# Performance work log

Measured on AMD Instinct MI355X. Metric: run time of the kernel, lower is better.

The kernel has to match this reference:

```python
import jax, jax.numpy as jnp
import numpy as np

N_NODES = 50000


def setup_inputs() -> dict:
    key = jax.random.key(0)
    k1, k2, k3, k4 = jax.random.split(key, 4)
    N, E, D_IN, D_OUT = N_NODES, 1_600_000, 128, 128
    x = jax.random.normal(k1, (N, D_IN), dtype=jnp.float32)
    edge_index = jax.random.randint(k2, (2, E), 0, N, dtype=jnp.int64)
    W = jax.random.normal(k3, (D_IN, D_OUT), dtype=jnp.float32) * (1.0 / np.sqrt(D_IN))
    b = jax.random.normal(k4, (D_OUT,), dtype=jnp.float32) * 0.01
    return {"x": x, "edge_index": edge_index, "W": W, "b": b}


def reference(x, edge_index, W, b):
    N = x.shape[0]
    # add self loops: edge (i, i) for every node
    loops = jnp.arange(N, dtype=edge_index.dtype)
    row = jnp.concatenate([edge_index[0], loops])  # [E+N]
    col = jnp.concatenate([edge_index[1], loops])  # [E+N]
    # degree over col (matches torch_geometric degree(col, N))
    deg = jax.ops.segment_sum(jnp.ones_like(col, dtype=x.dtype), col, num_segments=N)
    deg_inv_sqrt = jnp.where(deg > 0, jax.lax.rsqrt(jnp.maximum(deg, 1.0)), 0.0)
    norm = deg_inv_sqrt[row] * deg_inv_sqrt[col]  # [E+N]
    # linear transform then gather-multiply-scatter (segment sum over row)
    xl = x @ W + b  # [N, D_OUT]
    msg = norm[:, None] * xl[col]  # [E+N, D_OUT]
    out = jax.ops.segment_sum(msg, row, num_segments=N)
    return out
```

## Files before the change

kernel.cpp:

```cpp
#include <hip/hip_runtime.h>
#include <hip/hip_bf16.h>


#define D     128
#define TILE  8192
#define BINB  1024
#define RPB   64
#define CAPB  4096
#define MAXBK 1024
#define NH    256

typedef short  bf16x8 __attribute__((ext_vector_type(8)));
typedef float  f32x4  __attribute__((ext_vector_type(4)));
typedef unsigned short us4 __attribute__((ext_vector_type(4)));
typedef unsigned short us8 __attribute__((ext_vector_type(8)));

static __device__ __forceinline__ unsigned short f2bf(float f) {
    unsigned u = __float_as_uint(f);
    u = (u + 0x7FFFu + ((u >> 16) & 1u)) >> 16;
    return (unsigned short)u;
}
static __device__ __forceinline__ float bf2f(unsigned short s) {
    return __uint_as_float(((unsigned)s) << 16);
}

__global__ __launch_bounds__(256) void k_prep(const float* __restrict__ W,
                                              unsigned short* __restrict__ wtb,
                                              int* __restrict__ bcur,
                                              int NBK) {
    int i = blockIdx.x * 256 + threadIdx.x;
    if (i < NBK) bcur[i] = i * CAPB;
    if (i < D * D) {
        int n = i >> 7, k = i & 127;
        wtb[n * 128 + k] = f2bf(W[k * 128 + n]);
    }
}

__global__ __launch_bounds__(1024) void k_binjoint3(
        const int* __restrict__ rows, const int* __restrict__ cols,
        int* __restrict__ bcur, unsigned* __restrict__ ebuf,
        const float* __restrict__ x, const unsigned short* __restrict__ wtb,
        const float* __restrict__ bia, unsigned short* __restrict__ xlb,
        unsigned* __restrict__ phist,
        int E, int N, int NBK, int NT, int GN, int NW) {
    __shared__ __align__(16) unsigned char smem[65536];
    const int t = threadIdx.x;

    if ((int)blockIdx.x >= NT + GN) {
        unsigned* hist = (unsigned*)smem;
        for (int w = t; w < NW; w += BINB) hist[w] = 0;
        __syncthreads();
        const int hb   = (int)blockIdx.x - NT - GN;
        const int SEG  = (E + NH - 1) / NH;
        const int hbeg = hb * SEG;
        int hend = hbeg + SEG; if (hend > E) hend = E;
        for (int i = hbeg + t; i < hend; i += BINB) {
            unsigned c = (unsigned)cols[i];
            atomicAdd(&hist[c >> 2], 1u << ((c & 3u) * 8u));
        }
        __syncthreads();
        unsigned* dst = phist + (size_t)hb * NW;
        for (int w = t; w < NW; w += BINB) dst[w] = hist[w];
        return;
    }

    if ((int)blockIdx.x >= NT) {
        unsigned short (*wt)[136] = (unsigned short (*)[136])smem;
        unsigned short (*xs)[136] = (unsigned short (*)[136])(smem + 34816);
        const int row0 = ((int)blockIdx.x - NT) * 64;
        #pragma unroll
        for (int i = 0; i < 2; ++i) {
            int j = i * 1024 + t;
            int n = j >> 4, k8 = j & 15;
            us8 v = *(const us8*)&wtb[j * 8];
            *(us8*)&wt[n][k8 * 8] = v;
        }
        #pragma unroll
        for (int i = 0; i < 2; ++i) {
            int j = i * 1024 + t;
            int r = j >> 5, c4 = j & 31;
            int gr = row0 + r;
            us4 o = (us4){0, 0, 0, 0};
            if (gr < N) {
                float4 v = *(const float4*)&x[(size_t)gr * D + c4 * 4];
                o = (us4){f2bf(v.x), f2bf(v.y), f2bf(v.z), f2bf(v.w)};
            }
            *(us4*)&xs[r][c4 * 4] = o;
        }
        __syncthreads();
        if (t < 256) {
            const int w  = t >> 6, l = t & 63;
            const int m0 = w * 16;
            const int lm = l & 15, lq = l >> 4;
            f32x4 acc[8];
            #pragma unroll
            for (int nt = 0; nt < 8; ++nt) acc[nt] = (f32x4){0.f, 0.f, 0.f, 0.f};
            #pragma unroll
            for (int kk = 0; kk < 4; ++kk) {
                const int kof = kk * 32 + lq * 8;
                bf16x8 a = *(const bf16x8*)&xs[m0 + lm][kof];
                #pragma unroll
                for (int nt = 0; nt < 8; ++nt) {
                    bf16x8 bb = *(const bf16x8*)&wt[nt * 16 + lm][kof];
                    acc[nt] = __builtin_amdgcn_mfma_f32_16x16x32_bf16(a, bb, acc[nt], 0, 0, 0);
                }
            }
            #pragma unroll
            for (int nt = 0; nt < 8; ++nt) {
                const int col = nt * 16 + lm;
                const float bc = bia[col];
                #pragma unroll
                for (int r = 0; r < 4; ++r) {
                    int grow = row0 + m0 + lq * 4 + r;
                    if (grow < N) xlb[(size_t)grow * D + col] = f2bf(acc[nt][r] + bc);
                }
            }
        }
        return;
    }

    unsigned* sorted = (unsigned*)smem;
    int* lcnt  = (int*)(smem + 32768);
    int* lbase = lcnt + 800;
    int* excl  = lcnt + 1600;
    int* cur   = lcnt + 2400;

    const int base = blockIdx.x * TILE;
    int m = E - base; if (m > TILE) m = TILE;

    unsigned p[TILE / BINB];
    #pragma unroll
    for (int it = 0; it < TILE / BINB; ++it) {
        int i = it * BINB + t;
        if (i < m) {
            unsigned r = (unsigned)rows[base + i];
            unsigned c = (unsigned)cols[base + i];
            p[it] = c | ((r & 63u) << 16) | ((r >> 6) << 22);
        }
    }
    if (t < 800) lcnt[t] = 0;
    __syncthreads();
    #pragma unroll
    for (int it = 0; it < TILE / BINB; ++it) {
        int i = it * BINB + t;
        if (i < m) atomicAdd(&lcnt[p[it] >> 22], 1);
    }
    __syncthreads();
    if (t < 64) {
        int v[13], s = 0;
        #pragma unroll
        for (int u = 0; u < 13; ++u) {
            int k = t * 13 + u;
            v[u] = (k < NBK) ? lcnt[k] : 0;
            s += v[u];
        }
        int inc = s;
        #pragma unroll
        for (int off = 1; off < 64; off <<= 1) { int o = __shfl_up(inc, off); if (t >= off) inc += o; }
        int run = inc - s;
        #pragma unroll
        for (int u = 0; u < 13; ++u) {
            int k = t * 13 + u;
            if (k < NBK) { excl[k] = run; cur[k] = run; }
            run += v[u];
        }
    }
    if (t < NBK) {
        int c0 = lcnt[t];
        lbase[t] = c0 ? atomicAdd(&bcur[t], c0) : 0;
    }
    __syncthreads();
    #pragma unroll
    for (int it = 0; it < TILE / BINB; ++it) {
        int i = it * BINB + t;
        if (i < m) {
            int pos = atomicAdd(&cur[p[it] >> 22], 1);
            sorted[pos] = p[it];
        }
    }
    __syncthreads();
    #pragma unroll
    for (int it = 0; it < TILE / BINB; ++it) {
        int i = it * BINB + t;
        if (i < m) {
            unsigned pp = sorted[i];
            int bk = pp >> 22;
            int g  = lbase[bk] + i - excl[bk];
            if (g < (bk + 1) * CAPB) ebuf[g] = pp & 0x3FFFFFu;
        }
    }
}

__global__ __launch_bounds__(256) void k_dismerge(const unsigned* __restrict__ phist,
                                                  float* __restrict__ dis,
                                                  int N, int NW) {
    int w = blockIdx.x * 256 + threadIdx.x;
    if (w >= NW) return;
    unsigned s0 = 0, s1 = 0, s2 = 0, s3 = 0;
    const unsigned* pw = phist + w;
    #pragma unroll 8
    for (int b = 0; b < NH; ++b) {
        unsigned u = pw[(size_t)b * NW];
        s0 += u & 255u;
        s1 += (u >> 8) & 255u;
        s2 += (u >> 16) & 255u;
        s3 += u >> 24;
    }
    int c0 = w * 4;
    float4 o = make_float4(rsqrtf((float)(s0 + 1)), rsqrtf((float)(s1 + 1)),
                           rsqrtf((float)(s2 + 1)), rsqrtf((float)(s3 + 1)));
    if (c0 + 3 < N) {
        *(float4*)&dis[c0] = o;
    } else {
        if (c0     < N) dis[c0]     = o.x;
        if (c0 + 1 < N) dis[c0 + 1] = o.y;
        if (c0 + 2 < N) dis[c0 + 2] = o.z;
        if (c0 + 3 < N) dis[c0 + 3] = o.w;
    }
}

__global__ __launch_bounds__(512) void k_sortred2(const int* __restrict__ bcur,
                                                  const unsigned* __restrict__ ebuf,
                                                  const float* __restrict__ dis,
                                                  const unsigned short* __restrict__ xlb,
                                                  float* __restrict__ out, int N) {
    __shared__ unsigned short sorted[CAPB];
    __shared__ int cnt[RPB];
    __shared__ int excl[RPB];
    __shared__ int cur[RPB];
    const int t = threadIdx.x, b = blockIdx.x;
    const int ebase = b * CAPB;
    int m = bcur[b] - ebase;
    if (m > CAPB) m = CAPB;
    if (m < 0) m = 0;

    unsigned p[CAPB / 512];
    #pragma unroll
    for (int it = 0; it < CAPB / 512; ++it) {
        int i = it * 512 + t;
        p[it] = (i < m) ? ebuf[ebase + i] : 0xFFFFFFFFu;
    }
    if (t < RPB) cnt[t] = 0;
    __syncthreads();
    #pragma unroll
    for (int it = 0; it < CAPB / 512; ++it)
        if (p[it] != 0xFFFFFFFFu) atomicAdd(&cnt[(p[it] >> 16) & 63], 1);
    __syncthreads();
    if (t < 64) {
        int v = cnt[t], inc = v;
        #pragma unroll
        for (int off = 1; off < 64; off <<= 1) { int o = __shfl_up(inc, off); if (t >= off) inc += o; }
        excl[t] = inc - v;
        cur[t]  = inc - v;
    }
    __syncthreads();
    #pragma unroll
    for (int it = 0; it < CAPB / 512; ++it)
        if (p[it] != 0xFFFFFFFFu) {
            int pos = atomicAdd(&cur[(p[it] >> 16) & 63], 1);
            sorted[pos] = (unsigned short)(p[it] & 0xFFFFu);
        }
    __syncthreads();

    const int wv = t >> 6, lane = t & 63;
    const int half = lane >> 5, l32 = lane & 31;

#define FETCH(V, NN, J) do { \
    _Pragma("unroll") \
    for (int u = 0; u < 8; ++u) { \
        int idx = (J) + 2 * u + half; \
        int cc = __shfl(c, idx); \
        NN[u] = __shfl(n, idx); \
        V[u] = *(const us4*)&xlb[((size_t)cc << 7) + (l32 << 2)]; \
    } } while (0)
#define CONS(V, NN) do { \
    _Pragma("unroll") \
    for (int u = 0; u < 8; ++u) { \
        a0 = fmaf(NN[u], bf2f(V[u][0]), a0); \
        a1 = fmaf(NN[u], bf2f(V[u][1]), a1); \
        a2 = fmaf(NN[u], bf2f(V[u][2]), a2); \
        a3 = fmaf(NN[u], bf2f(V[u][3]), a3); \
    } } while (0)

    for (int r8 = 0; r8 < 8; ++r8) {
        const int rl = wv * 8 + r8;
        const int grow = b * RPB + rl;
        if (grow >= N) break;
        const float di = dis[grow];
        const int beg = excl[rl], end = cur[rl];
        us4 sv = *(const us4*)&xlb[(size_t)grow * D + (l32 << 2)];
        float s = (half == 0) ? di : 0.0f;
        float a0 = s * bf2f(sv[0]), a1 = s * bf2f(sv[1]);
        float a2 = s * bf2f(sv[2]), a3 = s * bf2f(sv[3]);
        for (int bs = beg; bs < end; bs += 64) {
            int mm = end - bs; if (mm > 64) mm = 64;
            int   c = 0;
            float n = 0.0f;
            if (lane < mm) {
                c = sorted[bs + lane];
                n = dis[c];
            }
            us4 A[8], B[8];
            float na[8], nb[8];
            int j = 0;
            FETCH(A, na, 0);
            for (; j + 32 <= mm; j += 32) {
                FETCH(B, nb, j + 16);
                CONS(A, na);
                if (j + 32 < mm) FETCH(A, na, j + 32);
                CONS(B, nb);
            }
            int rem = mm - j;
            if (rem > 0) {
                if (rem > 16) { FETCH(B, nb, j + 16); CONS(A, na); CONS(B, nb); }
                else          { CONS(A, na); }
            }
        }
        a0 += __shfl_xor(a0, 32);
        a1 += __shfl_xor(a1, 32);
        a2 += __shfl_xor(a2, 32);
        a3 += __shfl_xor(a3, 32);
        if (half == 0) {
            *(float4*)&out[(size_t)grow * D + (l32 << 2)] =
                make_float4(di * a0, di * a1, di * a2, di * a3);
        }
    }
#undef FETCH
#undef CONS
}

__global__ __launch_bounds__(256) void k_zero(int* __restrict__ p, int n) {
    int i = blockIdx.x * 256 + threadIdx.x;
    if (i < n) p[i] = 0;
}
__global__ __launch_bounds__(256) void k_deg(const int* __restrict__ cols,
                                             int* __restrict__ cntc, int E) {
    int e = blockIdx.x * 256 + threadIdx.x;
    if (e < E) atomicAdd(&cntc[cols[e]], 1);
}
__global__ __launch_bounds__(256) void k_dis(const int* __restrict__ cntc,
                                             float* __restrict__ dis, int N) {
    int i = blockIdx.x * 256 + threadIdx.x;
    if (i < N) dis[i] = rsqrtf((float)(cntc[i] + 1));
}
#define GEMM_R 8
__global__ __launch_bounds__(128) void k_gemmf(const float* __restrict__ x,
                                               const float* __restrict__ W,
                                               const float* __restrict__ b,
                                               float* __restrict__ xl, int N) {
    __shared__ float xs[GEMM_R][D];
    const int c  = threadIdx.x;
    const int r0 = blockIdx.x * GEMM_R;
    #pragma unroll
    for (int r = 0; r < GEMM_R; ++r) {
        int row = r0 + r;
        xs[r][c] = (row < N) ? x[row * D + c] : 0.0f;
    }
    __syncthreads();
    float acc[GEMM_R];
    const float bc = b[c];
    #pragma unroll
    for (int r = 0; r < GEMM_R; ++r) acc[r] = bc;
    for (int k = 0; k < D; k += 4) {
        const float w0 = W[(k + 0) * D + c];
        const float w1 = W[(k + 1) * D + c];
        const float w2 = W[(k + 2) * D + c];
        const float w3 = W[(k + 3) * D + c];
        #pragma unroll
        for (int r = 0; r < GEMM_R; ++r) {
            const float4 xv = *reinterpret_cast<const float4*>(&xs[r][k]);
            acc[r] = fmaf(xv.x, w0, acc[r]);
            acc[r] = fmaf(xv.y, w1, acc[r]);
            acc[r] = fmaf(xv.z, w2, acc[r]);
            acc[r] = fmaf(xv.w, w3, acc[r]);
        }
    }
    #pragma unroll
    for (int r = 0; r < GEMM_R; ++r) {
        int row = r0 + r;
        if (row < N) xl[row * D + c] = acc[r];
    }
}
__global__ __launch_bounds__(256) void k_self(const float* __restrict__ xl,
                                              const float* __restrict__ dis,
                                              float* __restrict__ out, int N) {
    int gid = blockIdx.x * 256 + threadIdx.x;
    int i = gid >> 7;
    if (i < N) {
        float d = dis[i];
        out[gid] = d * d * xl[gid];
    }
}
__global__ __launch_bounds__(256) void k_scatter(const int* __restrict__ rows,
                                                 const int* __restrict__ cols,
                                                 const float* __restrict__ dis,
                                                 const float* __restrict__ xl,
                                                 float* __restrict__ out, int E) {
    long long gid = (long long)blockIdx.x * 256 + threadIdx.x;
    int e    = (int)(gid >> 6);
    int lane = (int)(gid & 63);
    if (e >= E) return;
    const int row = rows[e];
    const int col = cols[e];
    const float nrm = dis[row] * dis[col];
    atomicAdd(&out[row * D + lane],      nrm * xl[col * D + lane]);
    atomicAdd(&out[row * D + 64 + lane], nrm * xl[col * D + 64 + lane]);
}

extern "C" void kernel_launch(void* const* d_in, const int* in_sizes, int n_in,
                              void* d_out, int out_size, void* d_ws, size_t ws_size,
                              hipStream_t stream) {
    const float* x   = (const float*)d_in[0];
    const int*   ei  = (const int*)d_in[1];
    const float* W   = (const float*)d_in[2];
    const float* b   = (const float*)d_in[3];
    float*       out = (float*)d_out;

    const int N = in_sizes[0] / D;
    const int E = in_sizes[1] / 2;
    const int* rows = ei;
    const int* cols = ei + E;
    const int NBK = (N + RPB - 1) / RPB;
    const int NT  = (E + TILE - 1) / TILE;
    const int GN  = (N + 63) / 64;
    const int NW  = (N + 3) / 4;

    char* p = (char*)d_ws;
    size_t off = 0;
    unsigned short* xlb     = (unsigned short*)(p + off); off += (size_t)N * D * 2;
    unsigned short* wtb     = (unsigned short*)(p + off); off += (size_t)D * D * 2;
    float*          dis     = (float*)(p + off);          off += (size_t)N * 4;
    int*            bcur    = (int*)(p + off);            off += (size_t)MAXBK * 4;
    unsigned*       ebuf    = (unsigned*)(p + off);       off += (size_t)NBK * CAPB * 4;
    unsigned*       phist   = (unsigned*)(p + off);       off += (size_t)NH * NW * 4;

    const int gN = (N + 255) / 256;
    const int gE = (E + 255) / 256;

    if (N <= 65536 && NBK <= MAXBK && ws_size >= off) {
        int gP = (D * D + 255) / 256;
        if (gP < (NBK + 255) / 256) gP = (NBK + 255) / 256;
        k_prep     <<<gP, 256, 0, stream>>>(W, wtb, bcur, NBK);
        k_binjoint3<<<NT + GN + NH, BINB, 0, stream>>>(rows, cols, bcur, ebuf,
                                                       x, wtb, b, xlb, phist,
                                                       E, N, NBK, NT, GN, NW);
        k_dismerge <<<(NW + 255) / 256, 256, 0, stream>>>(phist, dis, N, NW);
        k_sortred2 <<<NBK, 512, 0, stream>>>(bcur, ebuf, dis, xlb, out, N);
    } else {
        char* q = (char*)d_ws;
        float* xl   = (float*)q;
        float* disF = (float*)(q + (size_t)N * D * 4);
        int*   cc   = (int*)(q + (size_t)N * D * 4 + (size_t)N * 4);
        k_zero <<<gN, 256, 0, stream>>>(cc, N);
        k_deg  <<<gE, 256, 0, stream>>>(cols, cc, E);
        k_dis  <<<gN, 256, 0, stream>>>(cc, disF, N);
        k_gemmf<<<(N + GEMM_R - 1) / GEMM_R, 128, 0, stream>>>(x, W, b, xl, N);
        k_self <<<((N * D) + 255) / 256, 256, 0, stream>>>(xl, disF, out, N);
        long long st = (long long)E * 64;
        k_scatter<<<(int)((st + 255) / 256), 256, 0, stream>>>(rows, cols, disF, xl, out, E);
    }
}
```

Before: 194.7 us.

## Fold source-degree scaling into GEMM output and simplify reduction inner loop

The degree histogram is split into its own kernel and run before the binning/GEMM kernel, so the GEMM epilogue can multiply each xl row by deg^-1/2 of its source. The reduction kernel then sums pre-scaled bf16 rows with plain adds, reading column indices straight from LDS instead of shuffling them and gathering dis per edge, and applies the destination scale once at the end. Per-bucket atomic reservations are also rotated by block index to spread contention. In exchange the histogram no longer overlaps with binning and GEMM, since they now run as separate serialized launches, and scaling before bf16 rounding slightly changes numerics.

```diff
diff --git a/kernel.cpp b/kernel.cpp
--- a/kernel.cpp
+++ b/kernel.cpp
@@ -36,33 +36,63 @@
     }
 }
 
-__global__ __launch_bounds__(1024) void k_binjoint3(
+__global__ __launch_bounds__(1024) void k_hist(const int* __restrict__ cols,
+                                               unsigned* __restrict__ phist,
+                                               int E, int NW) {
+    __shared__ unsigned hist[16384];
+    const int t = threadIdx.x;
+    for (int w = t; w < NW; w += 1024) hist[w] = 0;
+    __syncthreads();
+    const int hb   = blockIdx.x;
+    const int SEG  = (E + NH - 1) / NH;
+    const int hbeg = hb * SEG;
+    int hend = hbeg + SEG; if (hend > E) hend = E;
+    for (int i = hbeg + t; i < hend; i += 1024) {
+        unsigned c = (unsigned)cols[i];
+        atomicAdd(&hist[c >> 2], 1u << ((c & 3u) * 8u));
+    }
+    __syncthreads();
+    unsigned* dst = phist + (size_t)hb * NW;
+    for (int w = t; w < NW; w += 1024) dst[w] = hist[w];
+}
+
+__global__ __launch_bounds__(256) void k_dismerge(const unsigned* __restrict__ phist,
+                                                  float* __restrict__ dis,
+                                                  int N, int NW) {
+    int w = blockIdx.x * 256 + threadIdx.x;
+    if (w >= NW) return;
+    unsigned s0 = 0, s1 = 0, s2 = 0, s3 = 0;
+    const unsigned* pw = phist + w;
+    #pragma unroll 8
+    for (int b = 0; b < NH; ++b) {
+        unsigned u = pw[(size_t)b * NW];
+        s0 += u & 255u;
+        s1 += (u >> 8) & 255u;
+        s2 += (u >> 16) & 255u;
+        s3 += u >> 24;
+    }
+    int c0 = w * 4;
+    float4 o = make_float4(rsqrtf((float)(s0 + 1)), rsqrtf((float)(s1 + 1)),
+                           rsqrtf((float)(s2 + 1)), rsqrtf((float)(s3 + 1)));
+    if (c0 + 3 < N) {
+        *(float4*)&dis[c0] = o;
+    } else {
+        if (c0     < N) dis[c0]     = o.x;
+        if (c0 + 1 < N) dis[c0 + 1] = o.y;
+        if (c0 + 2 < N) dis[c0 + 2] = o.z;
+        if (c0 + 3 < N) dis[c0 + 3] = o.w;
+    }
+}
+
+__global__ __launch_bounds__(1024) void k_binjoint4(
         const int* __restrict__ rows, const int* __restrict__ cols,
         int* __restrict__ bcur, unsigned* __restrict__ ebuf,
         const float* __restrict__ x, const unsigned short* __restrict__ wtb,
-        const float* __restrict__ bia, unsigned short* __restrict__ xlb,
-        unsigned* __restrict__ phist,
-        int E, int N, int NBK, int NT, int GN, int NW) {
+        const float* __restrict__ bia, const float* __restrict__ dis,
+        unsigned short* __restrict__ xlb,
+        int E, int N, int NBK, int NT) {
     __shared__ __align__(16) unsigned char smem[65536];
     const int t = threadIdx.x;
-
-    if ((int)blockIdx.x >= NT + GN) {
-        unsigned* hist = (unsigned*)smem;
-        for (int w = t; w < NW; w += BINB) hist[w] = 0;
-        __syncthreads();
-        const int hb   = (int)blockIdx.x - NT - GN;
-        const int SEG  = (E + NH - 1) / NH;
-        const int hbeg = hb * SEG;
-        int hend = hbeg + SEG; if (hend > E) hend = E;
-        for (int i = hbeg + t; i < hend; i += BINB) {
-            unsigned c = (unsigned)cols[i];
-            atomicAdd(&hist[c >> 2], 1u << ((c & 3u) * 8u));
-        }
-        __syncthreads();
-        unsigned* dst = phist + (size_t)hb * NW;
-        for (int w = t; w < NW; w += BINB) dst[w] = hist[w];
-        return;
-    }
 
     if ((int)blockIdx.x >= NT) {
         unsigned short (*wt)[136] = (unsigned short (*)[136])smem;
@@ -105,14 +135,17 @@
                     acc[nt] = __builtin_amdgcn_mfma_f32_16x16x32_bf16(a, bb, acc[nt], 0, 0, 0);
                 }
             }
+            float bc[8];
             #pragma unroll
-            for (int nt = 0; nt < 8; ++nt) {
-                const int col = nt * 16 + lm;
-                const float bc = bia[col];
-                #pragma unroll
-                for (int r = 0; r < 4; ++r) {
-                    int grow = row0 + m0 + lq * 4 + r;
-                    if (grow < N) xlb[(size_t)grow * D + col] = f2bf(acc[nt][r] + bc);
+            for (int nt = 0; nt < 8; ++nt) bc[nt] = bia[nt * 16 + lm];
+            #pragma unroll
+            for (int r = 0; r < 4; ++r) {
+                int grow = row0 + m0 + lq * 4 + r;
+                if (grow < N) {
+                    float dv = dis[grow];
+                    #pragma unroll
+                    for (int nt = 0; nt < 8; ++nt)
+                        xlb[(size_t)grow * D + nt * 16 + lm] = f2bf(dv * (acc[nt][r] + bc[nt]));
                 }
             }
         }
@@ -166,8 +199,10 @@
         }
     }
     if (t < NBK) {
-        int c0 = lcnt[t];
-        lbase[t] = c0 ? atomicAdd(&bcur[t], c0) : 0;
+        int tb = t + (int)((blockIdx.x * 331u) % (unsigned)NBK);
+        if (tb >= NBK) tb -= NBK;
+        int c0 = lcnt[tb];
+        lbase[tb] = c0 ? atomicAdd(&bcur[tb], c0) : 0;
     }
     __syncthreads();
     #pragma unroll
@@ -191,54 +226,25 @@
     }
 }
 
-__global__ __launch_bounds__(256) void k_dismerge(const unsigned* __restrict__ phist,
-                                                  float* __restrict__ dis,
-                                                  int N, int NW) {
-    int w = blockIdx.x * 256 + threadIdx.x;
-    if (w >= NW) return;
-    unsigned s0 = 0, s1 = 0, s2 = 0, s3 = 0;
-    const unsigned* pw = phist + w;
-    #pragma unroll 8
-    for (int b = 0; b < NH; ++b) {
-        unsigned u = pw[(size_t)b * NW];
-        s0 += u & 255u;
-        s1 += (u >> 8) & 255u;
-        s2 += (u >> 16) & 255u;
-        s3 += u >> 24;
-    }
-    int c0 = w * 4;
-    float4 o = make_float4(rsqrtf((float)(s0 + 1)), rsqrtf((float)(s1 + 1)),
-                           rsqrtf((float)(s2 + 1)), rsqrtf((float)(s3 + 1)));
-    if (c0 + 3 < N) {
-        *(float4*)&dis[c0] = o;
-    } else {
-        if (c0     < N) dis[c0]     = o.x;
-        if (c0 + 1 < N) dis[c0 + 1] = o.y;
-        if (c0 + 2 < N) dis[c0 + 2] = o.z;
-        if (c0 + 3 < N) dis[c0 + 3] = o.w;
-    }
-}
-
-__global__ __launch_bounds__(512) void k_sortred2(const int* __restrict__ bcur,
-                                                  const unsigned* __restrict__ ebuf,
-                                                  const float* __restrict__ dis,
-                                                  const unsigned short* __restrict__ xlb,
-                                                  float* __restrict__ out, int N) {
+__global__ __launch_bounds__(512, 8) void k_sortred3(
+        const int* __restrict__ bcur, const unsigned* __restrict__ ebuf,
+        const float* __restrict__ dis, const unsigned short* __restrict__ xlb,
+        float* __restrict__ out, int N) {
     __shared__ unsigned short sorted[CAPB];
     __shared__ int cnt[RPB];
     __shared__ int excl[RPB];
     __shared__ int cur[RPB];
     const int t = threadIdx.x, b = blockIdx.x;
     const int ebase = b * CAPB;
-    int m = bcur[b] - ebase;
-    if (m > CAPB) m = CAPB;
-    if (m < 0) m = 0;
+    int mb = bcur[b] - ebase;
+    if (mb > CAPB) mb = CAPB;
+    if (mb < 0) mb = 0;
 
     unsigned p[CAPB / 512];
     #pragma unroll
     for (int it = 0; it < CAPB / 512; ++it) {
         int i = it * 512 + t;
-        p[it] = (i < m) ? ebuf[ebase + i] : 0xFFFFFFFFu;
+        p[it] = (i < mb) ? ebuf[ebase + i] : 0xFFFFFFFFu;
     }
     if (t < RPB) cnt[t] = 0;
     __syncthreads();
@@ -265,55 +271,51 @@
     const int wv = t >> 6, lane = t & 63;
     const int half = lane >> 5, l32 = lane & 31;
 
-#define FETCH(V, NN, J) do { \
+#define FETCH(V, J) do { \
     _Pragma("unroll") \
     for (int u = 0; u < 8; ++u) { \
         int idx = (J) + 2 * u + half; \
-        int cc = __shfl(c, idx); \
-        NN[u] = __shfl(n, idx); \
+        int cc = sorted[beg + (idx < m ? idx : 0)]; \
         V[u] = *(const us4*)&xlb[((size_t)cc << 7) + (l32 << 2)]; \
     } } while (0)
-#define CONS(V, NN) do { \
+#define CFULL(V) do { \
     _Pragma("unroll") \
     for (int u = 0; u < 8; ++u) { \
-        a0 = fmaf(NN[u], bf2f(V[u][0]), a0); \
-        a1 = fmaf(NN[u], bf2f(V[u][1]), a1); \
-        a2 = fmaf(NN[u], bf2f(V[u][2]), a2); \
-        a3 = fmaf(NN[u], bf2f(V[u][3]), a3); \
+        a0 += bf2f(V[u][0]); a1 += bf2f(V[u][1]); \
+        a2 += bf2f(V[u][2]); a3 += bf2f(V[u][3]); \
+    } } while (0)
+#define CTAIL(V, J) do { \
+    _Pragma("unroll") \
+    for (int u = 0; u < 8; ++u) { \
+        float w = ((J) + 2 * u + half < m) ? 1.0f : 0.0f; \
+        a0 = fmaf(w, bf2f(V[u][0]), a0); a1 = fmaf(w, bf2f(V[u][1]), a1); \
+        a2 = fmaf(w, bf2f(V[u][2]), a2); a3 = fmaf(w, bf2f(V[u][3]), a3); \
     } } while (0)
 
     for (int r8 = 0; r8 < 8; ++r8) {
         const int rl = wv * 8 + r8;
         const int grow = b * RPB + rl;
         if (grow >= N) break;
-        const float di = dis[grow];
-        const int beg = excl[rl], end = cur[rl];
+        const int beg = excl[rl];
+        const int m = cur[rl] - beg;
         us4 sv = *(const us4*)&xlb[(size_t)grow * D + (l32 << 2)];
-        float s = (half == 0) ? di : 0.0f;
+        float s = (half == 0) ? 1.0f : 0.0f;
         float a0 = s * bf2f(sv[0]), a1 = s * bf2f(sv[1]);
         float a2 = s * bf2f(sv[2]), a3 = s * bf2f(sv[3]);
-        for (int bs = beg; bs < end; bs += 64) {
-            int mm = end - bs; if (mm > 64) mm = 64;
-            int   c = 0;
-            float n = 0.0f;
-            if (lane < mm) {
-                c = sorted[bs + lane];
-                n = dis[c];
+        if (m > 0) {
+            us4 A[8], B[8];
+            int j = 0;
+            FETCH(A, 0);
+            for (; j + 32 <= m; j += 32) {
+                FETCH(B, j + 16);
+                CFULL(A);
+                if (j + 32 < m) FETCH(A, j + 32);
+                CFULL(B);
             }
-            us4 A[8], B[8];
-            float na[8], nb[8];
-            int j = 0;
-            FETCH(A, na, 0);
-            for (; j + 32 <= mm; j += 32) {
-                FETCH(B, nb, j + 16);
-                CONS(A, na);
-                if (j + 32 < mm) FETCH(A, na, j + 32);
-                CONS(B, nb);
-            }
-            int rem = mm - j;
+            int rem = m - j;
             if (rem > 0) {
-                if (rem > 16) { FETCH(B, nb, j + 16); CONS(A, na); CONS(B, nb); }
-                else          { CONS(A, na); }
+                if (rem > 16) { FETCH(B, j + 16); CFULL(A); CTAIL(B, j + 16); }
+                else          { CTAIL(A, j); }
             }
         }
         a0 += __shfl_xor(a0, 32);
@@ -321,12 +323,14 @@
         a2 += __shfl_xor(a2, 32);
         a3 += __shfl_xor(a3, 32);
         if (half == 0) {
+            const float di = dis[grow];
             *(float4*)&out[(size_t)grow * D + (l32 << 2)] =
                 make_float4(di * a0, di * a1, di * a2, di * a3);
         }
     }
 #undef FETCH
-#undef CONS
+#undef CFULL
+#undef CTAIL
 }
 
 __global__ __launch_bounds__(256) void k_zero(int* __restrict__ p, int n) {
@@ -437,15 +441,16 @@
     const int gN = (N + 255) / 256;
     const int gE = (E + 255) / 256;
 
-    if (N <= 65536 && NBK <= MAXBK && ws_size >= off) {
+    if (N <= 65536 && NBK <= MAXBK && NBK <= 800 && ws_size >= off) {
         int gP = (D * D + 255) / 256;
         if (gP < (NBK + 255) / 256) gP = (NBK + 255) / 256;
         k_prep     <<<gP, 256, 0, stream>>>(W, wtb, bcur, NBK);
-        k_binjoint3<<<NT + GN + NH, BINB, 0, stream>>>(rows, cols, bcur, ebuf,
-                                                       x, wtb, b, xlb, phist,
-                                                       E, N, NBK, NT, GN, NW);
+        k_hist     <<<NH, 1024, 0, stream>>>(cols, phist, E, NW);
         k_dismerge <<<(NW + 255) / 256, 256, 0, stream>>>(phist, dis, N, NW);
-        k_sortred2 <<<NBK, 512, 0, stream>>>(bcur, ebuf, dis, xlb, out, N);
+        k_binjoint4<<<NT + GN, BINB, 0, stream>>>(rows, cols, bcur, ebuf,
+                                                  x, wtb, b, dis, xlb,
+                                                  E, N, NBK, NT);
+        k_sortred3 <<<NBK, 512, 0, stream>>>(bcur, ebuf, dis, xlb, out, N);
     } else {
         char* q = (char*)d_ws;
         float* xl   = (float*)q;
```

Measured after the change: 228.5 us. +17.4%, slower.
